# Kernel optimization log

Hardware: AMD Instinct MI355X
Metric: run time of the kernel (lower is better)

The kernel has to match this reference:

```python
import jax, jax.numpy as jnp
import numpy as np

B, C, L = 64, 512, 4096


def setup_inputs() -> dict:
    key = jax.random.key(0)
    x = jax.random.normal(key, (B, C, L), dtype=jnp.float32)
    return {"x": x}


def reference(x) -> jnp.ndarray:
    # x: [B, C, L]. Module attends across the B axis, batched over L.
    b, c, l = x.shape
    q = jnp.transpose(x, (2, 0, 1))               # [L, B, C] (query = key = value)
    scale = jnp.asarray(c, x.dtype) ** 0.5
    # scores[l, n, m] = <q[l, n, :], q[l, m, :]> / sqrt(C)   -> [L, B, B]
    scores = jnp.einsum('lnc,lmc->lnm', q, q) / scale
    prob = jax.nn.softmax(scores, axis=-1)
    msg = jnp.einsum('lnm,lmc->lnc', prob, q)     # [L, B, C]
    return x + jnp.transpose(msg, (1, 2, 0))      # [B, C, L]
```

## Files before the change

### kernel.cpp

```cpp
#include <hip/hip_runtime.h>

typedef __bf16 bf16x8 __attribute__((ext_vector_type(8)));
typedef float  f32x4  __attribute__((ext_vector_type(4)));

#define NB 64
#define NC 512
#define NL 4096
#define LT 16


__global__ __launch_bounds__(512, 2)
void attn_prop_kernel(const float* __restrict__ x, float* __restrict__ out)
{
    __shared__ __align__(16) unsigned char smem_raw[131072];
    __bf16* const p_lds = (__bf16*)smem_raw;
    __bf16* const s1    = (__bf16*)smem_raw;
    __bf16* const s2    = (__bf16*)smem_raw;

    const int tid  = threadIdx.x;
    const int wave = tid >> 6;
    const int lane = tid & 63;
    const int quad = lane >> 4;
    const int c16  = lane & 15;
    const int l0   = blockIdx.x * LT;

    f32x4 acc[2][4][4];
#pragma unroll
    for (int ll = 0; ll < 2; ++ll)
#pragma unroll
        for (int i = 0; i < 4; ++i)
#pragma unroll
            for (int j = 0; j < 4; ++j)
                acc[ll][i][j] = (f32x4){0.f, 0.f, 0.f, 0.f};

    for (int kc = 0; kc < 16; ++kc) {
        const int c0 = kc * 32;
        __syncthreads();
#pragma unroll
        for (int r = 0; r < 4; ++r) {
            const int m  = (tid >> 5) + (r << 4);
            const int cc = tid & 31;
            const float* src = x + ((m * NC + c0 + cc) * NL + l0);
            union { float4 q[4]; float f[16]; } u;
            u.q[0] = ((const float4*)src)[0];
            u.q[1] = ((const float4*)src)[1];
            u.q[2] = ((const float4*)src)[2];
            u.q[3] = ((const float4*)src)[3];
#pragma unroll
            for (int l = 0; l < 16; ++l)
                s1[(l * 64 + m) * 40 + cc] = (__bf16)u.f[l];
        }
        __syncthreads();
#pragma unroll
        for (int ll = 0; ll < 2; ++ll) {
            const int l = wave * 2 + ll;
            bf16x8 a[4];
#pragma unroll
            for (int i = 0; i < 4; ++i)
                a[i] = *(const bf16x8*)(s1 + (l * 64 + i * 16 + c16) * 40 + quad * 8);
#pragma unroll
            for (int i = 0; i < 4; ++i)
#pragma unroll
                for (int j = 0; j < 4; ++j)
                    acc[ll][i][j] = __builtin_amdgcn_mfma_f32_16x16x32_bf16(
                        a[i], a[j], acc[ll][i][j], 0, 0, 0);
        }
    }
    __syncthreads();

    const float rs = 0.04419417382415922f;
#pragma unroll
    for (int ll = 0; ll < 2; ++ll) {
        const int l = wave * 2 + ll;
#pragma unroll
        for (int i = 0; i < 4; ++i) {
#pragma unroll
            for (int q = 0; q < 4; ++q) {
                float s[4];
#pragma unroll
                for (int j = 0; j < 4; ++j) s[j] = acc[ll][i][j][q] * rs;
                float rmax = fmaxf(fmaxf(s[0], s[1]), fmaxf(s[2], s[3]));
#pragma unroll
                for (int d = 1; d <= 8; d <<= 1)
                    rmax = fmaxf(rmax, __shfl_xor(rmax, d, 64));
                float e[4], rsum = 0.f;
#pragma unroll
                for (int j = 0; j < 4; ++j) { e[j] = __expf(s[j] - rmax); rsum += e[j]; }
#pragma unroll
                for (int d = 1; d <= 8; d <<= 1)
                    rsum += __shfl_xor(rsum, d, 64);
                const float inv = 1.0f / rsum;
                const int n = i * 16 + quad * 4 + q;
#pragma unroll
                for (int j = 0; j < 4; ++j) {
                    float p = e[j] * inv;
                    if (i == j && (quad * 4 + q) == c16) p += 1.0f;
                    p_lds[l * 4096 + n * 64 + j * 16 + c16] = (__bf16)p;
                }
            }
        }
    }
    __syncthreads();

    const int iw = wave & 3;
    const int jw = wave >> 2;
    bf16x8 pf[16][2];
#pragma unroll
    for (int l = 0; l < 16; ++l)
#pragma unroll
        for (int k2 = 0; k2 < 2; ++k2)
            pf[l][k2] = *(const bf16x8*)(p_lds + l * 4096 + (iw * 16 + c16) * 64 + k2 * 32 + quad * 8);
    __syncthreads();

    for (int ch = 0; ch < 16; ++ch) {
        const int c0 = ch * 32;
#pragma unroll
        for (int r = 0; r < 4; ++r) {
            const int m  = tid & 63;
            const int cc = (tid >> 6) + (r << 3);
            const float* src = x + ((m * NC + c0 + cc) * NL + l0);
            union { float4 q[4]; float f[16]; } u;
            u.q[0] = ((const float4*)src)[0];
            u.q[1] = ((const float4*)src)[1];
            u.q[2] = ((const float4*)src)[2];
            u.q[3] = ((const float4*)src)[3];
#pragma unroll
            for (int l = 0; l < 16; ++l)
                s2[cc * 1032 + l * 64 + m] = (__bf16)u.f[l];
        }
        __syncthreads();

        f32x4 acc2[16];
#pragma unroll
        for (int l = 0; l < 16; ++l) {
            f32x4 a2 = (f32x4){0.f, 0.f, 0.f, 0.f};
#pragma unroll
            for (int k2 = 0; k2 < 2; ++k2) {
                bf16x8 b = *(const bf16x8*)(s2 + (jw * 16 + c16) * 1032 + l * 64 + k2 * 32 + quad * 8);
                a2 = __builtin_amdgcn_mfma_f32_16x16x32_bf16(pf[l][k2], b, a2, 0, 0, 0);
            }
            acc2[l] = a2;
        }

        const int cg = c0 + jw * 16 + c16;
#pragma unroll
        for (int q = 0; q < 4; ++q) {
            const int n = iw * 16 + quad * 4 + q;
            float* dst = out + ((n * NC + cg) * NL + l0);
            float4 w;
            w.x = acc2[0][q];  w.y = acc2[1][q];  w.z = acc2[2][q];  w.w = acc2[3][q];
            ((float4*)dst)[0] = w;
            w.x = acc2[4][q];  w.y = acc2[5][q];  w.z = acc2[6][q];  w.w = acc2[7][q];
            ((float4*)dst)[1] = w;
            w.x = acc2[8][q];  w.y = acc2[9][q];  w.z = acc2[10][q]; w.w = acc2[11][q];
            ((float4*)dst)[2] = w;
            w.x = acc2[12][q]; w.y = acc2[13][q]; w.z = acc2[14][q]; w.w = acc2[15][q];
            ((float4*)dst)[3] = w;
        }
        __syncthreads();
    }
}

extern "C" void kernel_launch(void* const* d_in, const int* in_sizes, int n_in,
                              void* d_out, int out_size, void* d_ws, size_t ws_size,
                              hipStream_t stream)
{
    const float* x = (const float*)d_in[0];
    float* o = (float*)d_out;
    attn_prop_kernel<<<dim3(NL / LT), dim3(512), 0, stream>>>(x, o);
}
```

Baseline: 1.376 ms.

## Register-prefetch next x chunk during MFMA phases and remap global loads

Global loads of x are moved into a 16-float4 register buffer that is filled for the next channel chunk while the current chunk is converted into LDS and consumed by MFMAs, in both the QK^T and PV phases. The load mapping changes so four consecutive threads read one 64-byte row segment, which coalesces better. The PV accumulator is split into two halves of 8 so the larger prefetch buffer fits in registers. In exchange, register pressure rises with launch bounds (512,2), and the LDS write pattern changes, which may cause bank conflicts.

```diff
diff --git a/kernel.cpp b/kernel.cpp
--- a/kernel.cpp
+++ b/kernel.cpp
@@ -24,6 +24,9 @@
     const int c16  = lane & 15;
     const int l0   = blockIdx.x * LT;
 
+    const int srow = tid >> 2;
+    const int seg  = tid & 3;
+
     f32x4 acc[2][4][4];
 #pragma unroll
     for (int ll = 0; ll < 2; ++ll)
@@ -33,22 +36,33 @@
             for (int j = 0; j < 4; ++j)
                 acc[ll][i][j] = (f32x4){0.f, 0.f, 0.f, 0.f};
 
+    float4 R[16];
+
+#pragma unroll
+    for (int r = 0; r < 16; ++r) {
+        const int row = (r << 7) + srow;
+        const int m = row >> 5, cc = row & 31;
+        R[r] = *(const float4*)(x + ((m * NC + cc) * NL + l0) + (seg << 2));
+    }
+
     for (int kc = 0; kc < 16; ++kc) {
-        const int c0 = kc * 32;
         __syncthreads();
 #pragma unroll
-        for (int r = 0; r < 4; ++r) {
-            const int m  = (tid >> 5) + (r << 4);
-            const int cc = tid & 31;
-            const float* src = x + ((m * NC + c0 + cc) * NL + l0);
-            union { float4 q[4]; float f[16]; } u;
-            u.q[0] = ((const float4*)src)[0];
-            u.q[1] = ((const float4*)src)[1];
-            u.q[2] = ((const float4*)src)[2];
-            u.q[3] = ((const float4*)src)[3];
+        for (int r = 0; r < 16; ++r) {
+            const int row = (r << 7) + srow;
+            const int m = row >> 5, cc = row & 31;
 #pragma unroll
-            for (int l = 0; l < 16; ++l)
-                s1[(l * 64 + m) * 40 + cc] = (__bf16)u.f[l];
+            for (int j = 0; j < 4; ++j)
+                s1[((seg * 4 + j) * 64 + m) * 40 + cc] = (__bf16)R[r][j];
+        }
+        if (kc < 15) {
+            const int c0n = (kc + 1) * 32;
+#pragma unroll
+            for (int r = 0; r < 16; ++r) {
+                const int row = (r << 7) + srow;
+                const int m = row >> 5, cc = row & 31;
+                R[r] = *(const float4*)(x + ((m * NC + c0n + cc) * NL + l0) + (seg << 2));
+            }
         }
         __syncthreads();
 #pragma unroll
@@ -66,6 +80,14 @@
                         a[i], a[j], acc[ll][i][j], 0, 0, 0);
         }
     }
+
+#pragma unroll
+    for (int r = 0; r < 16; ++r) {
+        const int row = (r << 7) + srow;
+        const int m = row >> 5, cc = row & 31;
+        R[r] = *(const float4*)(x + ((m * NC + cc) * NL + l0) + (seg << 2));
+    }
+
     __syncthreads();
 
     const float rs = 0.04419417382415922f;
@@ -113,49 +135,51 @@
     __syncthreads();
 
     for (int ch = 0; ch < 16; ++ch) {
-        const int c0 = ch * 32;
 #pragma unroll
-        for (int r = 0; r < 4; ++r) {
-            const int m  = tid & 63;
-            const int cc = (tid >> 6) + (r << 3);
-            const float* src = x + ((m * NC + c0 + cc) * NL + l0);
-            union { float4 q[4]; float f[16]; } u;
-            u.q[0] = ((const float4*)src)[0];
-            u.q[1] = ((const float4*)src)[1];
-            u.q[2] = ((const float4*)src)[2];
-            u.q[3] = ((const float4*)src)[3];
+        for (int r = 0; r < 16; ++r) {
+            const int row = (r << 7) + srow;
+            const int m = row >> 5, cc = row & 31;
 #pragma unroll
-            for (int l = 0; l < 16; ++l)
-                s2[cc * 1032 + l * 64 + m] = (__bf16)u.f[l];
+            for (int j = 0; j < 4; ++j)
+                s2[cc * 1032 + (seg * 4 + j) * 64 + m] = (__bf16)R[r][j];
+        }
+        if (ch < 15) {
+            const int c0n = (ch + 1) * 32;
+#pragma unroll
+            for (int r = 0; r < 16; ++r) {
+                const int row = (r << 7) + srow;
+                const int m = row >> 5, cc = row & 31;
+                R[r] = *(const float4*)(x + ((m * NC + c0n + cc) * NL + l0) + (seg << 2));
+            }
         }
         __syncthreads();
 
-        f32x4 acc2[16];
-#pragma unroll
-        for (int l = 0; l < 16; ++l) {
-            f32x4 a2 = (f32x4){0.f, 0.f, 0.f, 0.f};
-#pragma unroll
-            for (int k2 = 0; k2 < 2; ++k2) {
-                bf16x8 b = *(const bf16x8*)(s2 + (jw * 16 + c16) * 1032 + l * 64 + k2 * 32 + quad * 8);
-                a2 = __builtin_amdgcn_mfma_f32_16x16x32_bf16(pf[l][k2], b, a2, 0, 0, 0);
-            }
-            acc2[l] = a2;
-        }
-
+        const int c0 = ch * 32;
         const int cg = c0 + jw * 16 + c16;
 #pragma unroll
-        for (int q = 0; q < 4; ++q) {
-            const int n = iw * 16 + quad * 4 + q;
-            float* dst = out + ((n * NC + cg) * NL + l0);
-            float4 w;
-            w.x = acc2[0][q];  w.y = acc2[1][q];  w.z = acc2[2][q];  w.w = acc2[3][q];
-            ((float4*)dst)[0] = w;
-            w.x = acc2[4][q];  w.y = acc2[5][q];  w.z = acc2[6][q];  w.w = acc2[7][q];
-            ((float4*)dst)[1] = w;
-            w.x = acc2[8][q];  w.y = acc2[9][q];  w.z = acc2[10][q]; w.w = acc2[11][q];
-            ((float4*)dst)[2] = w;
-            w.x = acc2[12][q]; w.y = acc2[13][q]; w.z = acc2[14][q]; w.w = acc2[15][q];
-            ((float4*)dst)[3] = w;
+        for (int h = 0; h < 2; ++h) {
+            f32x4 acc2[8];
+#pragma unroll
+            for (int u = 0; u < 8; ++u) {
+                const int l = h * 8 + u;
+                f32x4 a2 = (f32x4){0.f, 0.f, 0.f, 0.f};
+#pragma unroll
+                for (int k2 = 0; k2 < 2; ++k2) {
+                    bf16x8 b = *(const bf16x8*)(s2 + (jw * 16 + c16) * 1032 + l * 64 + k2 * 32 + quad * 8);
+                    a2 = __builtin_amdgcn_mfma_f32_16x16x32_bf16(pf[l][k2], b, a2, 0, 0, 0);
+                }
+                acc2[u] = a2;
+            }
+#pragma unroll
+            for (int q = 0; q < 4; ++q) {
+                const int n = iw * 16 + quad * 4 + q;
+                float* dst = out + ((n * NC + cg) * NL + l0) + h * 8;
+                float4 w;
+                w.x = acc2[0][q]; w.y = acc2[1][q]; w.z = acc2[2][q]; w.w = acc2[3][q];
+                ((float4*)dst)[0] = w;
+                w.x = acc2[4][q]; w.y = acc2[5][q]; w.z = acc2[6][q]; w.w = acc2[7][q];
+                ((float4*)dst)[1] = w;
+            }
         }
         __syncthreads();
     }
```

Result: no change. 1.364 ms (-0.9%).
